# Kernel optimization log

Hardware: AMD Instinct MI355X
Metric: run time of the kernel (lower is better)

## Reference

```python
import jax, jax.numpy as jnp
import numpy as np

N = 1024      # number of atoms
L = 64        # latent_size
VOCAB = 20    # vocab_size (len(ATOM_CATEGORIES))


def _lin(key, fan_in, fan_out):
    # mimic torch nn.Linear init: U(-1/sqrt(fan_in), 1/sqrt(fan_in))
    kw, kb = jax.random.split(key)
    s = 1.0 / np.sqrt(fan_in)
    W = jax.random.uniform(kw, (fan_in, fan_out), minval=-s, maxval=s, dtype=jnp.float32)
    b = jax.random.uniform(kb, (fan_out,), minval=-s, maxval=s, dtype=jnp.float32)
    return W, b


def setup_inputs() -> dict:
    key = jax.random.key(0)
    ks = jax.random.split(key, 9)
    We1, be1 = _lin(ks[3], 2 * L + 1, L)   # mlp_e layer 1
    We2, be2 = _lin(ks[4], L, L)           # mlp_e layer 2
    Wh1, bh1 = _lin(ks[5], L + 1, L)       # mlp_h layer 1
    Wh2, bh2 = _lin(ks[6], L, L)           # mlp_h layer 2
    Wo, bo = _lin(ks[7], L, 1)             # output_mlp
    return {
        "atom_categories": jax.random.randint(ks[0], (N,), 0, VOCAB),
        "atom_coordinates": jax.random.normal(ks[1], (N, 3), dtype=jnp.float32),
        "learnable_matrix": jax.random.normal(ks[2], (VOCAB, L), dtype=jnp.float32),
        "We1": We1, "be1": be1, "We2": We2, "be2": be2,
        "Wh1": Wh1, "bh1": bh1, "Wh2": Wh2, "bh2": bh2,
        "Wo": Wo, "bo": bo,
    }


def reference(atom_categories, atom_coordinates, learnable_matrix,
              We1, be1, We2, be2, Wh1, bh1, Wh2, bh2, Wo, bo):
    Z = atom_coordinates
    # init_H: learnable_matrix.T @ one_hot(cat) == row gather
    H = learnable_matrix[atom_categories]                       # [N, L]

    # pairwise squared distances ||Z_i - Z_j||^2
    d2 = jnp.sum((Z[:, None, :] - Z[None, :, :]) ** 2, axis=-1)  # [N, N]

    # mlp_e layer 1 on concat(H_i, H_j, d2): split We1 to avoid materializing concat
    W1i, W1j, w1z = We1[:L], We1[L:2 * L], We1[2 * L]            # [L,L],[L,L],[L]
    pre_i = H @ W1i                                              # [N, L]
    pre_j = H @ W1j                                              # [N, L]
    h1 = jnp.tanh(pre_i[:, None, :] + pre_j[None, :, :]
                  + d2[:, :, None] * w1z + be1)                  # [N, N, L]
    W_e = jnp.tanh(h1 @ We2 + be2)                               # [N, N, L]

    # V[i] = sum over j != i of sum_l W_e[i,j,l]
    total = jnp.sum(W_e, axis=(1, 2))                            # [N]
    diag = jnp.einsum('iil->i', W_e)                             # [N]
    V = total - diag                                             # [N]

    # mlp_h on concat(H_i, V_i): split Wh1
    hh = jnp.tanh(H @ Wh1[:L] + V[:, None] * Wh1[L] + bh1)       # [N, L]
    newH = jnp.tanh(hh @ Wh2 + bh2)                              # [N, L]

    Hsum = jnp.sum(newH, axis=0)                                 # [L]
    return (Hsum @ Wo + bo)[0]                                   # scalar
```

## Files before the change

### kernel.cpp

```cpp
#include <hip/hip_runtime.h>
#include <hip/hip_bf16.h>


#define N_ATOMS 1024
#define L_DIM 64
#define CSCALE 2.8853900817779268f

typedef _Float16 f16x8 __attribute__((ext_vector_type(8)));
typedef __fp16  fp16x2 __attribute__((ext_vector_type(2)));
typedef float f32x4 __attribute__((ext_vector_type(4)));

__device__ __forceinline__ float tanh_fast(float x) {
    float e = __builtin_amdgcn_exp2f(x * CSCALE);
    float r = __builtin_amdgcn_rcpf(e + 1.0f);
    return fmaf(-2.0f, r, 1.0f);
}

__global__ __launch_bounds__(256) void k_prep(const int* __restrict__ cat,
                                              const float* __restrict__ LM,
                                              const float* __restrict__ We1,
                                              const float* __restrict__ be1,
                                              const float* __restrict__ We2,
                                              const float* __restrict__ be2,
                                              float* __restrict__ H,
                                              float* __restrict__ preI,
                                              float* __restrict__ P3,
                                              float* __restrict__ Vpart,
                                              f16x8* __restrict__ bHg,
                                              f16x8* __restrict__ bLg,
                                              float* __restrict__ biasg,
                                              float* __restrict__ out) {
    int t = threadIdx.x;
    int sub = t >> 6, l = t & 63;
    int i = blockIdx.x * 4 + sub;
    if (blockIdx.x == 0 && t == 0) out[0] = 0.f;
    if (t < 4) Vpart[blockIdx.x * 4 + t] = 0.f;
    __shared__ float hrow[4][L_DIM];
    float hv = LM[cat[i] * L_DIM + l];
    hrow[sub][l] = hv;
    H[i * L_DIM + l] = hv;
    __syncthreads();
    float s1 = 0.f, s2 = 0.f;
#pragma unroll
    for (int m = 0; m < L_DIM; m++) {
        float h = hrow[sub][m];
        s1 = fmaf(h, We1[m * L_DIM + l], s1);
        s2 = fmaf(h, We1[(L_DIM + m) * L_DIM + l], s2);
    }
    preI[i * L_DIM + l] = s1 * CSCALE;
    int cc = i >> 4;
    int Ll = i & 15;
    int quad = (l >> 3) & 3;
    int L = quad * 16 + Ll;
    int g = ((l >> 5) << 1) | ((l >> 2) & 1);
    int e2 = l & 3;
    P3[cc * 1024 + g * 256 + L * 4 + e2] = (s2 + be1[l]) * CSCALE;

    if (blockIdx.x == 0) {
        int nt = t >> 6;
        int lane = t & 63;
        int q2 = lane >> 4, nl2 = lane & 15;
        float psum = 0.f;
#pragma unroll
        for (int kt = 0; kt < 2; kt++) {
            f16x8 hi8, lo8;
#pragma unroll
            for (int e = 0; e < 8; e++) {
                float x = We2[(kt * 32 + q2 * 8 + e) * L_DIM + nt * 16 + nl2];
                psum += x;
                float wp = -2.0f * CSCALE * x;
                _Float16 hi = (_Float16)wp;
                hi8[e] = hi;
                lo8[e] = (_Float16)(wp - (float)hi);
            }
            bHg[(kt * 4 + nt) * 64 + lane] = hi8;
            bLg[(kt * 4 + nt) * 64 + lane] = lo8;
        }
        psum += __shfl_xor(psum, 16);
        psum += __shfl_xor(psum, 32);
        biasg[lane * 4 + nt] = CSCALE * (be2[nt * 16 + nl2] + psum);
    }
}

__global__ __launch_bounds__(256) void k_main(const float* __restrict__ Z,
                                              const float* __restrict__ We1,
                                              const float* __restrict__ preI,
                                              const float* __restrict__ P3,
                                              const f16x8* __restrict__ bHg,
                                              const f16x8* __restrict__ bLg,
                                              const float* __restrict__ biasg,
                                              float* __restrict__ Vpart) {
    int bid = blockIdx.x;
    int i = bid >> 1, half = bid & 1;
    int t = threadIdx.x;
    int lane = t & 63;
    int wave = t >> 6;
    int nlo = lane & 15;
    int quad = lane >> 4;

    __shared__ float d2s[512];
    __shared__ float red[256];
    __shared__ f16x8 bLs[8 * 64];

    float zi0 = Z[i * 3], zi1 = Z[i * 3 + 1], zi2 = Z[i * 3 + 2];
    for (int p = t; p < 512; p += 256) {
        int j = half * 512 + p;
        float a = zi0 - Z[j * 3], b = zi1 - Z[j * 3 + 1], c = zi2 - Z[j * 3 + 2];
        d2s[p] = a * a + b * b + c * c;
    }

    f32x4 aiR[4], wzR[4];
#pragma unroll
    for (int g = 0; g < 4; g++) {
        int mb = ((g >> 1) << 5) + (quad << 3) + ((g & 1) << 2);
        aiR[g] = *(const f32x4*)(preI + i * L_DIM + mb);
        f32x4 wz = *(const f32x4*)(We1 + 2 * L_DIM * L_DIM + mb);
        wzR[g] = wz * CSCALE;
    }

    f16x8 bH[4][2];
#pragma unroll
    for (int nt = 0; nt < 4; nt++) {
        bH[nt][0] = bHg[(0 * 4 + nt) * 64 + lane];
        bH[nt][1] = bHg[(1 * 4 + nt) * 64 + lane];
    }
#pragma unroll
    for (int idx = 0; idx < 2; idx++) {
        int e = wave + idx * 4;
        bLs[e * 64 + lane] = bLg[e * 64 + lane];
    }
    f32x4 bias4 = *(const f32x4*)(biasg + lane * 4);

    const float* Pbase = P3 + (half * 32 + wave * 8) * 1024 + lane * 4;
    f32x4 p0 = *(const f32x4*)(Pbase + 0 * 256) + aiR[0];
    f32x4 p1 = *(const f32x4*)(Pbase + 1 * 256) + aiR[1];
    f32x4 p2 = *(const f32x4*)(Pbase + 2 * 256) + aiR[2];
    f32x4 p3 = *(const f32x4*)(Pbase + 3 * 256) + aiR[3];

    __syncthreads();

    f32x4 Vr4 = {0.f, 0.f, 0.f, 0.f};
    for (int k = 0; k < 8; k++) {
        float d2 = d2s[(wave * 8 + k) * 16 + nlo];
        f32x4 d2v = {d2, d2, d2, d2};

        f32x4 z0 = p0 + d2v * wzR[0];
        f32x4 z1 = p1 + d2v * wzR[1];
        f32x4 z2 = p2 + d2v * wzR[2];
        f32x4 z3 = p3 + d2v * wzR[3];
        f32x4 ex0, ex1, ex2, ex3;
#pragma unroll
        for (int e = 0; e < 4; e++) {
            ex0[e] = __builtin_amdgcn_exp2f(z0[e]);
            ex1[e] = __builtin_amdgcn_exp2f(z1[e]);
            ex2[e] = __builtin_amdgcn_exp2f(z2[e]);
            ex3[e] = __builtin_amdgcn_exp2f(z3[e]);
        }
        ex0 += 1.0f; ex1 += 1.0f; ex2 += 1.0f; ex3 += 1.0f;
        f32x4 r0, r1, r2, r3;
#pragma unroll
        for (int e = 0; e < 4; e++) {
            r0[e] = __builtin_amdgcn_rcpf(ex0[e]);
            r1[e] = __builtin_amdgcn_rcpf(ex1[e]);
            r2[e] = __builtin_amdgcn_rcpf(ex2[e]);
            r3[e] = __builtin_amdgcn_rcpf(ex3[e]);
        }
        union { f16x8 v; fp16x2 h2[4]; } u0, u1;
        u0.h2[0] = __builtin_amdgcn_cvt_pkrtz(r0[0], r0[1]);
        u0.h2[1] = __builtin_amdgcn_cvt_pkrtz(r0[2], r0[3]);
        u0.h2[2] = __builtin_amdgcn_cvt_pkrtz(r1[0], r1[1]);
        u0.h2[3] = __builtin_amdgcn_cvt_pkrtz(r1[2], r1[3]);
        u1.h2[0] = __builtin_amdgcn_cvt_pkrtz(r2[0], r2[1]);
        u1.h2[1] = __builtin_amdgcn_cvt_pkrtz(r2[2], r2[3]);
        u1.h2[2] = __builtin_amdgcn_cvt_pkrtz(r3[0], r3[1]);
        u1.h2[3] = __builtin_amdgcn_cvt_pkrtz(r3[2], r3[3]);
        f16x8 aH0 = u0.v, aH1 = u1.v;

        if (k < 7) {
            const float* nb = Pbase + (k + 1) * 1024;
            p0 = *(const f32x4*)(nb + 0 * 256) + aiR[0];
            p1 = *(const f32x4*)(nb + 1 * 256) + aiR[1];
            p2 = *(const f32x4*)(nb + 2 * 256) + aiR[2];
            p3 = *(const f32x4*)(nb + 3 * 256) + aiR[3];
        }

#pragma unroll
        for (int nt = 0; nt < 4; nt++) {
            f16x8 bl0 = bLs[(0 * 4 + nt) * 64 + lane];
            f16x8 bl1 = bLs[(1 * 4 + nt) * 64 + lane];
            f32x4 acc = {bias4[nt], bias4[nt], bias4[nt], bias4[nt]};
            acc = __builtin_amdgcn_mfma_f32_16x16x32_f16(aH0, bH[nt][0], acc, 0, 0, 0);
            acc = __builtin_amdgcn_mfma_f32_16x16x32_f16(aH0, bl0, acc, 0, 0, 0);
            acc = __builtin_amdgcn_mfma_f32_16x16x32_f16(aH1, bH[nt][1], acc, 0, 0, 0);
            acc = __builtin_amdgcn_mfma_f32_16x16x32_f16(aH1, bl1, acc, 0, 0, 0);
            f32x4 ev;
#pragma unroll
            for (int r4 = 0; r4 < 4; r4++) ev[r4] = __builtin_amdgcn_exp2f(acc[r4]);
            ev += 1.0f;
            f32x4 rv;
#pragma unroll
            for (int r4 = 0; r4 < 4; r4++) rv[r4] = __builtin_amdgcn_rcpf(ev[r4]);
            Vr4 += rv;
        }
    }

    red[t] = Vr4[0] + Vr4[1] + Vr4[2] + Vr4[3];
    __syncthreads();
    if (t < 64) {
        float r = red[t] + red[t + 64] + red[t + 128] + red[t + 192];
#pragma unroll
        for (int o = 32; o > 0; o >>= 1) r += __shfl_xor(r, o);
        if (t == 0) atomicAdd(Vpart + i, r);
    }
}

__global__ __launch_bounds__(256) void k_post(const float* __restrict__ preI,
                                              const float* __restrict__ P3,
                                              const float* __restrict__ H,
                                              const float* __restrict__ We2,
                                              const float* __restrict__ be2,
                                              const float* __restrict__ Wh1,
                                              const float* __restrict__ bh1,
                                              const float* __restrict__ Wh2,
                                              const float* __restrict__ bh2,
                                              const float* __restrict__ Wo,
                                              const float* __restrict__ bo,
                                              const float* __restrict__ Vpart,
                                              float* __restrict__ out) {
    int t = threadIdx.x;
    int sub = t >> 6, lane = t & 63;
    int i = blockIdx.x * 4 + sub;
    __shared__ float dgt[4][L_DIM];
    __shared__ float hrow_s[4][L_DIM];
    __shared__ float hh_s[4][L_DIM];

    float Rall = Vpart[i];
    int cc = i >> 4, Ll = i & 15;
    int q2 = (lane >> 3) & 3;
    int g = ((lane >> 5) << 1) | ((lane >> 2) & 1);
    float z = preI[i * L_DIM + lane] + P3[cc * 1024 + g * 256 + (q2 * 16 + Ll) * 4 + (lane & 3)];
    float rr = __builtin_amdgcn_rcpf(__builtin_amdgcn_exp2f(z) + 1.0f);
    dgt[sub][lane] = fmaf(-2.0f, rr, 1.0f);
    hrow_s[sub][lane] = H[i * L_DIM + lane];
    __syncthreads();

    float S = be2[lane];
#pragma unroll
    for (int m = 0; m < L_DIM; m++) S = fmaf(dgt[sub][m], We2[m * L_DIM + lane], S);
    float rd = __builtin_amdgcn_rcpf(__builtin_amdgcn_exp2f(S * CSCALE) + 1.0f);
#pragma unroll
    for (int o = 32; o > 0; o >>= 1) rd += __shfl_xor(rd, o);
    float V = fmaf(-2.0f, Rall - rd, (float)(1023 * L_DIM));
    float s = 0.f;
#pragma unroll
    for (int m = 0; m < L_DIM; m++) s = fmaf(hrow_s[sub][m], Wh1[m * L_DIM + lane], s);
    s = fmaf(V, Wh1[L_DIM * L_DIM + lane], s) + bh1[lane];
    hh_s[sub][lane] = tanh_fast(s);
    __syncthreads();

    float s2 = 0.f;
#pragma unroll
    for (int m = 0; m < L_DIM; m++) s2 = fmaf(hh_s[sub][m], Wh2[m * L_DIM + lane], s2);
    float nh = tanh_fast(s2 + bh2[lane]);
    float w = nh * Wo[lane];
#pragma unroll
    for (int o = 32; o > 0; o >>= 1) w += __shfl_down(w, o);
    if (lane == 0) atomicAdd(out, w + (i == 0 ? bo[0] : 0.f));
}

extern "C" void kernel_launch(void* const* d_in, const int* in_sizes, int n_in,
                              void* d_out, int out_size, void* d_ws, size_t ws_size,
                              hipStream_t stream) {
    const int*   cat = (const int*)  d_in[0];
    const float* Z   = (const float*)d_in[1];
    const float* LM  = (const float*)d_in[2];
    const float* We1 = (const float*)d_in[3];
    const float* be1 = (const float*)d_in[4];
    const float* We2 = (const float*)d_in[5];
    const float* be2 = (const float*)d_in[6];
    const float* Wh1 = (const float*)d_in[7];
    const float* bh1 = (const float*)d_in[8];
    const float* Wh2 = (const float*)d_in[9];
    const float* bh2 = (const float*)d_in[10];
    const float* Wo  = (const float*)d_in[11];
    const float* bo  = (const float*)d_in[12];
    float* out = (float*)d_out;

    float* ws    = (float*)d_ws;
    float* H     = ws;
    float* preI  = H     + N_ATOMS * L_DIM;
    float* P3    = preI  + N_ATOMS * L_DIM;
    float* Vpart = P3    + N_ATOMS * L_DIM;
    float* biasg = Vpart + N_ATOMS;
    f16x8* bHg   = (f16x8*)(biasg + 256);
    f16x8* bLg   = bHg + 8 * 64;

    k_prep<<<N_ATOMS / 4, 256, 0, stream>>>(cat, LM, We1, be1, We2, be2,
                                            H, preI, P3, Vpart, bHg, bLg, biasg, out);
    k_main<<<N_ATOMS * 2, 256, 0, stream>>>(Z, We1, preI, P3, bHg, bLg, biasg, Vpart);
    k_post<<<N_ATOMS / 4, 256, 0, stream>>>(preI, P3, H, We2, be2,
                                            Wh1, bh1, Wh2, bh2, Wo, bo, Vpart, out);
}
```

Before: 137.3 us.

## Fuse main and post kernels via last-block-done counter, use per-category projection table

Replaces the three-kernel pipeline with a tiny setup kernel plus one fused kernel. The per-atom j-side projection is rebuilt as a 20-row per-category table in shared memory, indexed by atom category, instead of a 1024-row global P3 array. The per-atom MLP tail now runs in whichever of the two half-blocks finishes second, detected with an atomic done counter, which removes the k_post launch. In exchange every block recomputes the category table and the i-side projection (about 1.3K FMAs per thread of redundant work), and correctness relies on atomics and threadfence ordering.

New measurement: 239.7 us. 74.5% more time.

```diff
diff --git a/kernel.cpp b/kernel.cpp
--- a/kernel.cpp
+++ b/kernel.cpp
@@ -5,6 +5,7 @@
 #define N_ATOMS 1024
 #define L_DIM 64
 #define CSCALE 2.8853900817779268f
+#define T2LD 68
 
 typedef _Float16 f16x8 __attribute__((ext_vector_type(8)));
 typedef __fp16  fp16x2 __attribute__((ext_vector_type(2)));
@@ -16,46 +17,15 @@
     return fmaf(-2.0f, r, 1.0f);
 }
 
-__global__ __launch_bounds__(256) void k_prep(const int* __restrict__ cat,
-                                              const float* __restrict__ LM,
-                                              const float* __restrict__ We1,
-                                              const float* __restrict__ be1,
-                                              const float* __restrict__ We2,
+__global__ __launch_bounds__(256) void k_pre0(const float* __restrict__ We2,
                                               const float* __restrict__ be2,
-                                              float* __restrict__ H,
-                                              float* __restrict__ preI,
-                                              float* __restrict__ P3,
-                                              float* __restrict__ Vpart,
                                               f16x8* __restrict__ bHg,
                                               f16x8* __restrict__ bLg,
                                               float* __restrict__ biasg,
+                                              float* __restrict__ Vpart,
+                                              int* __restrict__ done,
                                               float* __restrict__ out) {
     int t = threadIdx.x;
-    int sub = t >> 6, l = t & 63;
-    int i = blockIdx.x * 4 + sub;
-    if (blockIdx.x == 0 && t == 0) out[0] = 0.f;
-    if (t < 4) Vpart[blockIdx.x * 4 + t] = 0.f;
-    __shared__ float hrow[4][L_DIM];
-    float hv = LM[cat[i] * L_DIM + l];
-    hrow[sub][l] = hv;
-    H[i * L_DIM + l] = hv;
-    __syncthreads();
-    float s1 = 0.f, s2 = 0.f;
-#pragma unroll
-    for (int m = 0; m < L_DIM; m++) {
-        float h = hrow[sub][m];
-        s1 = fmaf(h, We1[m * L_DIM + l], s1);
-        s2 = fmaf(h, We1[(L_DIM + m) * L_DIM + l], s2);
-    }
-    preI[i * L_DIM + l] = s1 * CSCALE;
-    int cc = i >> 4;
-    int Ll = i & 15;
-    int quad = (l >> 3) & 3;
-    int L = quad * 16 + Ll;
-    int g = ((l >> 5) << 1) | ((l >> 2) & 1);
-    int e2 = l & 3;
-    P3[cc * 1024 + g * 256 + L * 4 + e2] = (s2 + be1[l]) * CSCALE;
-
     if (blockIdx.x == 0) {
         int nt = t >> 6;
         int lane = t & 63;
@@ -79,17 +49,33 @@
         psum += __shfl_xor(psum, 16);
         psum += __shfl_xor(psum, 32);
         biasg[lane * 4 + nt] = CSCALE * (be2[nt * 16 + nl2] + psum);
+        if (t == 0) out[0] = 0.f;
+    } else {
+        int idx = (blockIdx.x - 1) * 256 + t;
+        if (idx < N_ATOMS) Vpart[idx] = 0.f;
+        else done[idx - N_ATOMS] = 0;
     }
 }
 
-__global__ __launch_bounds__(256) void k_main(const float* __restrict__ Z,
-                                              const float* __restrict__ We1,
-                                              const float* __restrict__ preI,
-                                              const float* __restrict__ P3,
-                                              const f16x8* __restrict__ bHg,
-                                              const f16x8* __restrict__ bLg,
-                                              const float* __restrict__ biasg,
-                                              float* __restrict__ Vpart) {
+__global__ __launch_bounds__(256) void k_fused(const int* __restrict__ cat,
+                                               const float* __restrict__ Z,
+                                               const float* __restrict__ LM,
+                                               const float* __restrict__ We1,
+                                               const float* __restrict__ be1,
+                                               const float* __restrict__ We2,
+                                               const float* __restrict__ be2,
+                                               const f16x8* __restrict__ bHg,
+                                               const f16x8* __restrict__ bLg,
+                                               const float* __restrict__ biasg,
+                                               const float* __restrict__ Wh1,
+                                               const float* __restrict__ bh1,
+                                               const float* __restrict__ Wh2,
+                                               const float* __restrict__ bh2,
+                                               const float* __restrict__ Wo,
+                                               const float* __restrict__ bo,
+                                               float* __restrict__ Vpart,
+                                               int* __restrict__ done,
+                                               float* __restrict__ out) {
     int bid = blockIdx.x;
     int i = bid >> 1, half = bid & 1;
     int t = threadIdx.x;
@@ -101,21 +87,38 @@
     __shared__ float d2s[512];
     __shared__ float red[256];
     __shared__ f16x8 bLs[8 * 64];
+    __shared__ float T2s[20 * T2LD];
+    __shared__ float preIs[L_DIM];
+    __shared__ int   cats[512];
+    __shared__ float dgt[L_DIM];
+    __shared__ float hhs[L_DIM];
+    __shared__ float RallS;
+    __shared__ int   winflag;
 
     float zi0 = Z[i * 3], zi1 = Z[i * 3 + 1], zi2 = Z[i * 3 + 2];
     for (int p = t; p < 512; p += 256) {
         int j = half * 512 + p;
+        cats[p] = cat[j];
         float a = zi0 - Z[j * 3], b = zi1 - Z[j * 3 + 1], c = zi2 - Z[j * 3 + 2];
         d2s[p] = a * a + b * b + c * c;
     }
 
-    f32x4 aiR[4], wzR[4];
-#pragma unroll
-    for (int g = 0; g < 4; g++) {
-        int mb = ((g >> 1) << 5) + (quad << 3) + ((g & 1) << 2);
-        aiR[g] = *(const f32x4*)(preI + i * L_DIM + mb);
-        f32x4 wz = *(const f32x4*)(We1 + 2 * L_DIM * L_DIM + mb);
-        wzR[g] = wz * CSCALE;
+#pragma unroll
+    for (int r = 0; r < 5; r++) {
+        int c = wave + 4 * r;
+        float s = 0.f;
+#pragma unroll
+        for (int m = 0; m < L_DIM; m++)
+            s = fmaf(LM[c * L_DIM + m], We1[(L_DIM + m) * L_DIM + lane], s);
+        T2s[c * T2LD + lane] = (s + be1[lane]) * CSCALE;
+    }
+    int ci = cat[i];
+    if (t < 64) {
+        float s = 0.f;
+#pragma unroll
+        for (int m = 0; m < L_DIM; m++)
+            s = fmaf(LM[ci * L_DIM + m], We1[m * L_DIM + t], s);
+        preIs[t] = s * CSCALE;
     }
 
     f16x8 bH[4][2];
@@ -131,13 +134,33 @@
     }
     f32x4 bias4 = *(const f32x4*)(biasg + lane * 4);
 
-    const float* Pbase = P3 + (half * 32 + wave * 8) * 1024 + lane * 4;
-    f32x4 p0 = *(const f32x4*)(Pbase + 0 * 256) + aiR[0];
-    f32x4 p1 = *(const f32x4*)(Pbase + 1 * 256) + aiR[1];
-    f32x4 p2 = *(const f32x4*)(Pbase + 2 * 256) + aiR[2];
-    f32x4 p3 = *(const f32x4*)(Pbase + 3 * 256) + aiR[3];
+    int mbs[4];
+    f32x4 wzR[4];
+#pragma unroll
+    for (int g = 0; g < 4; g++) {
+        int mb = ((g >> 1) << 5) + (quad << 3) + ((g & 1) << 2);
+        mbs[g] = mb;
+        f32x4 wz = *(const f32x4*)(We1 + 2 * L_DIM * L_DIM + mb);
+        wzR[g] = wz * CSCALE;
+    }
 
     __syncthreads();
+
+    f32x4 aiR[4];
+#pragma unroll
+    for (int g = 0; g < 4; g++) aiR[g] = *(const f32x4*)(preIs + mbs[g]);
+
+    {
+        int sc = cats[(wave * 8 + 0) * 16 + nlo];
+        const float* Tr = T2s + sc * T2LD;
+        (void)Tr;
+    }
+    int sc0 = cats[(wave * 8) * 16 + nlo];
+    const float* Tr0 = T2s + sc0 * T2LD;
+    f32x4 p0 = *(const f32x4*)(Tr0 + mbs[0]) + aiR[0];
+    f32x4 p1 = *(const f32x4*)(Tr0 + mbs[1]) + aiR[1];
+    f32x4 p2 = *(const f32x4*)(Tr0 + mbs[2]) + aiR[2];
+    f32x4 p3 = *(const f32x4*)(Tr0 + mbs[3]) + aiR[3];
 
     f32x4 Vr4 = {0.f, 0.f, 0.f, 0.f};
     for (int k = 0; k < 8; k++) {
@@ -177,11 +200,12 @@
         f16x8 aH0 = u0.v, aH1 = u1.v;
 
         if (k < 7) {
-            const float* nb = Pbase + (k + 1) * 1024;
-            p0 = *(const f32x4*)(nb + 0 * 256) + aiR[0];
-            p1 = *(const f32x4*)(nb + 1 * 256) + aiR[1];
-            p2 = *(const f32x4*)(nb + 2 * 256) + aiR[2];
-            p3 = *(const f32x4*)(nb + 3 * 256) + aiR[3];
+            int sc = cats[(wave * 8 + k + 1) * 16 + nlo];
+            const float* Tr = T2s + sc * T2LD;
+            p0 = *(const f32x4*)(Tr + mbs[0]) + aiR[0];
+            p1 = *(const f32x4*)(Tr + mbs[1]) + aiR[1];
+            p2 = *(const f32x4*)(Tr + mbs[2]) + aiR[2];
+            p3 = *(const f32x4*)(Tr + mbs[3]) + aiR[3];
         }
 
 #pragma unroll
@@ -206,66 +230,59 @@
 
     red[t] = Vr4[0] + Vr4[1] + Vr4[2] + Vr4[3];
     __syncthreads();
+
     if (t < 64) {
         float r = red[t] + red[t + 64] + red[t + 128] + red[t + 192];
 #pragma unroll
         for (int o = 32; o > 0; o >>= 1) r += __shfl_xor(r, o);
-        if (t == 0) atomicAdd(Vpart + i, r);
-    }
-}
-
-__global__ __launch_bounds__(256) void k_post(const float* __restrict__ preI,
-                                              const float* __restrict__ P3,
-                                              const float* __restrict__ H,
-                                              const float* __restrict__ We2,
-                                              const float* __restrict__ be2,
-                                              const float* __restrict__ Wh1,
-                                              const float* __restrict__ bh1,
-                                              const float* __restrict__ Wh2,
-                                              const float* __restrict__ bh2,
-                                              const float* __restrict__ Wo,
-                                              const float* __restrict__ bo,
-                                              const float* __restrict__ Vpart,
-                                              float* __restrict__ out) {
-    int t = threadIdx.x;
-    int sub = t >> 6, lane = t & 63;
-    int i = blockIdx.x * 4 + sub;
-    __shared__ float dgt[4][L_DIM];
-    __shared__ float hrow_s[4][L_DIM];
-    __shared__ float hh_s[4][L_DIM];
-
-    float Rall = Vpart[i];
-    int cc = i >> 4, Ll = i & 15;
-    int q2 = (lane >> 3) & 3;
-    int g = ((lane >> 5) << 1) | ((lane >> 2) & 1);
-    float z = preI[i * L_DIM + lane] + P3[cc * 1024 + g * 256 + (q2 * 16 + Ll) * 4 + (lane & 3)];
-    float rr = __builtin_amdgcn_rcpf(__builtin_amdgcn_exp2f(z) + 1.0f);
-    dgt[sub][lane] = fmaf(-2.0f, rr, 1.0f);
-    hrow_s[sub][lane] = H[i * L_DIM + lane];
+        if (t == 0) {
+            atomicAdd(Vpart + i, r);
+            __threadfence();
+            int old = atomicAdd(done + i, 1);
+            if (old == 1) {
+                __threadfence();
+                RallS = atomicAdd(Vpart + i, 0.0f);
+                winflag = 1;
+            } else {
+                winflag = 0;
+            }
+        }
+    }
     __syncthreads();
 
-    float S = be2[lane];
-#pragma unroll
-    for (int m = 0; m < L_DIM; m++) S = fmaf(dgt[sub][m], We2[m * L_DIM + lane], S);
-    float rd = __builtin_amdgcn_rcpf(__builtin_amdgcn_exp2f(S * CSCALE) + 1.0f);
-#pragma unroll
-    for (int o = 32; o > 0; o >>= 1) rd += __shfl_xor(rd, o);
-    float V = fmaf(-2.0f, Rall - rd, (float)(1023 * L_DIM));
-    float s = 0.f;
-#pragma unroll
-    for (int m = 0; m < L_DIM; m++) s = fmaf(hrow_s[sub][m], Wh1[m * L_DIM + lane], s);
-    s = fmaf(V, Wh1[L_DIM * L_DIM + lane], s) + bh1[lane];
-    hh_s[sub][lane] = tanh_fast(s);
-    __syncthreads();
-
-    float s2 = 0.f;
-#pragma unroll
-    for (int m = 0; m < L_DIM; m++) s2 = fmaf(hh_s[sub][m], Wh2[m * L_DIM + lane], s2);
-    float nh = tanh_fast(s2 + bh2[lane]);
-    float w = nh * Wo[lane];
-#pragma unroll
-    for (int o = 32; o > 0; o >>= 1) w += __shfl_down(w, o);
-    if (lane == 0) atomicAdd(out, w + (i == 0 ? bo[0] : 0.f));
+    if (winflag) {
+        if (t < 64) {
+            float z = preIs[t] + T2s[ci * T2LD + t];
+            float rr = __builtin_amdgcn_rcpf(__builtin_amdgcn_exp2f(z) + 1.0f);
+            dgt[t] = fmaf(-2.0f, rr, 1.0f);
+        }
+        __syncthreads();
+        if (t < 64) {
+            float S = be2[t];
+#pragma unroll
+            for (int m = 0; m < L_DIM; m++) S = fmaf(dgt[m], We2[m * L_DIM + t], S);
+            float rd = __builtin_amdgcn_rcpf(__builtin_amdgcn_exp2f(S * CSCALE) + 1.0f);
+#pragma unroll
+            for (int o = 32; o > 0; o >>= 1) rd += __shfl_xor(rd, o);
+            float V = fmaf(-2.0f, RallS - rd, (float)(1023 * L_DIM));
+            float s = 0.f;
+#pragma unroll
+            for (int m = 0; m < L_DIM; m++) s = fmaf(LM[ci * L_DIM + m], Wh1[m * L_DIM + t], s);
+            s = fmaf(V, Wh1[L_DIM * L_DIM + t], s) + bh1[t];
+            hhs[t] = tanh_fast(s);
+        }
+        __syncthreads();
+        if (t < 64) {
+            float s2 = 0.f;
+#pragma unroll
+            for (int m = 0; m < L_DIM; m++) s2 = fmaf(hhs[m], Wh2[m * L_DIM + t], s2);
+            float nh = tanh_fast(s2 + bh2[t]);
+            float w = nh * Wo[t];
+#pragma unroll
+            for (int o = 32; o > 0; o >>= 1) w += __shfl_down(w, o);
+            if (t == 0) atomicAdd(out, w + (i == 0 ? bo[0] : 0.f));
+        }
+    }
 }
 
 extern "C" void kernel_launch(void* const* d_in, const int* in_sizes, int n_in,
@@ -287,17 +304,15 @@
     float* out = (float*)d_out;
 
     float* ws    = (float*)d_ws;
-    float* H     = ws;
-    float* preI  = H     + N_ATOMS * L_DIM;
-    float* P3    = preI  + N_ATOMS * L_DIM;
-    float* Vpart = P3    + N_ATOMS * L_DIM;
-    float* biasg = Vpart + N_ATOMS;
-    f16x8* bHg   = (f16x8*)(biasg + 256);
+    float* Vpart = ws;
+    int*   done  = (int*)(ws + N_ATOMS);
+    float* biasg = ws + 2 * N_ATOMS;
+    f16x8* bHg   = (f16x8*)(ws + 2 * N_ATOMS + 256);
     f16x8* bLg   = bHg + 8 * 64;
 
-    k_prep<<<N_ATOMS / 4, 256, 0, stream>>>(cat, LM, We1, be1, We2, be2,
-                                            H, preI, P3, Vpart, bHg, bLg, biasg, out);
-    k_main<<<N_ATOMS * 2, 256, 0, stream>>>(Z, We1, preI, P3, bHg, bLg, biasg, Vpart);
-    k_post<<<N_ATOMS / 4, 256, 0, stream>>>(preI, P3, H, We2, be2,
-                                            Wh1, bh1, Wh2, bh2, Wo, bo, Vpart, out);
+    k_pre0<<<9, 256, 0, stream>>>(We2, be2, bHg, bLg, biasg, Vpart, done, out);
+    k_fused<<<N_ATOMS * 2, 256, 0, stream>>>(cat, Z, LM, We1, be1, We2, be2,
+                                             bHg, bLg, biasg,
+                                             Wh1, bh1, Wh2, bh2, Wo, bo,
+                                             Vpart, done, out);
 }
```

## Fuse post-processing into main kernel via last-block-done atomic counter

Applied to the files above, without the earlier changes.

Removes the k_post launch by having the second of two blocks finishing each atom (detected with an atomic done counter after a threadfence) run the per-atom mlp_h and output reduction inside k_main. This saves one kernel launch and its tail/launch gap. In exchange it adds atomics and a fence per block, a serial tail of one-wave work on the winning block, and extra shared memory and registers in k_main that could lower occupancy.

New measurement: 150.8 us. 1.1x slower.

```diff
diff --git a/kernel.cpp b/kernel.cpp
--- a/kernel.cpp
+++ b/kernel.cpp
@@ -26,6 +26,7 @@
                                               float* __restrict__ preI,
                                               float* __restrict__ P3,
                                               float* __restrict__ Vpart,
+                                              int* __restrict__ done,
                                               f16x8* __restrict__ bHg,
                                               f16x8* __restrict__ bLg,
                                               float* __restrict__ biasg,
@@ -34,7 +35,10 @@
     int sub = t >> 6, l = t & 63;
     int i = blockIdx.x * 4 + sub;
     if (blockIdx.x == 0 && t == 0) out[0] = 0.f;
-    if (t < 4) Vpart[blockIdx.x * 4 + t] = 0.f;
+    if (t < 4) {
+        Vpart[blockIdx.x * 4 + t] = 0.f;
+        done[blockIdx.x * 4 + t] = 0;
+    }
     __shared__ float hrow[4][L_DIM];
     float hv = LM[cat[i] * L_DIM + l];
     hrow[sub][l] = hv;
@@ -89,7 +93,18 @@
                                               const f16x8* __restrict__ bHg,
                                               const f16x8* __restrict__ bLg,
                                               const float* __restrict__ biasg,
-                                              float* __restrict__ Vpart) {
+                                              const float* __restrict__ H,
+                                              const float* __restrict__ We2,
+                                              const float* __restrict__ be2,
+                                              const float* __restrict__ Wh1,
+                                              const float* __restrict__ bh1,
+                                              const float* __restrict__ Wh2,
+                                              const float* __restrict__ bh2,
+                                              const float* __restrict__ Wo,
+                                              const float* __restrict__ bo,
+                                              float* __restrict__ Vpart,
+                                              int* __restrict__ done,
+                                              float* __restrict__ out) {
     int bid = blockIdx.x;
     int i = bid >> 1, half = bid & 1;
     int t = threadIdx.x;
@@ -101,6 +116,11 @@
     __shared__ float d2s[512];
     __shared__ float red[256];
     __shared__ f16x8 bLs[8 * 64];
+    __shared__ float dgt[L_DIM];
+    __shared__ float hrow_s[L_DIM];
+    __shared__ float hhs[L_DIM];
+    __shared__ float RallS;
+    __shared__ int   winflag;
 
     float zi0 = Z[i * 3], zi1 = Z[i * 3 + 1], zi2 = Z[i * 3 + 2];
     for (int p = t; p < 512; p += 256) {
@@ -206,66 +226,62 @@
 
     red[t] = Vr4[0] + Vr4[1] + Vr4[2] + Vr4[3];
     __syncthreads();
+
     if (t < 64) {
         float r = red[t] + red[t + 64] + red[t + 128] + red[t + 192];
 #pragma unroll
         for (int o = 32; o > 0; o >>= 1) r += __shfl_xor(r, o);
-        if (t == 0) atomicAdd(Vpart + i, r);
-    }
-}
-
-__global__ __launch_bounds__(256) void k_post(const float* __restrict__ preI,
-                                              const float* __restrict__ P3,
-                                              const float* __restrict__ H,
-                                              const float* __restrict__ We2,
-                                              const float* __restrict__ be2,
-                                              const float* __restrict__ Wh1,
-                                              const float* __restrict__ bh1,
-                                              const float* __restrict__ Wh2,
-                                              const float* __restrict__ bh2,
-                                              const float* __restrict__ Wo,
-                                              const float* __restrict__ bo,
-                                              const float* __restrict__ Vpart,
-                                              float* __restrict__ out) {
-    int t = threadIdx.x;
-    int sub = t >> 6, lane = t & 63;
-    int i = blockIdx.x * 4 + sub;
-    __shared__ float dgt[4][L_DIM];
-    __shared__ float hrow_s[4][L_DIM];
-    __shared__ float hh_s[4][L_DIM];
-
-    float Rall = Vpart[i];
-    int cc = i >> 4, Ll = i & 15;
-    int q2 = (lane >> 3) & 3;
-    int g = ((lane >> 5) << 1) | ((lane >> 2) & 1);
-    float z = preI[i * L_DIM + lane] + P3[cc * 1024 + g * 256 + (q2 * 16 + Ll) * 4 + (lane & 3)];
-    float rr = __builtin_amdgcn_rcpf(__builtin_amdgcn_exp2f(z) + 1.0f);
-    dgt[sub][lane] = fmaf(-2.0f, rr, 1.0f);
-    hrow_s[sub][lane] = H[i * L_DIM + lane];
+        if (t == 0) {
+            atomicAdd(Vpart + i, r);
+            __threadfence();
+            int old = atomicAdd(done + i, 1);
+            if (old == 1) {
+                RallS = atomicAdd(Vpart + i, 0.0f);
+                winflag = 1;
+            } else {
+                winflag = 0;
+            }
+        }
+    }
     __syncthreads();
 
-    float S = be2[lane];
-#pragma unroll
-    for (int m = 0; m < L_DIM; m++) S = fmaf(dgt[sub][m], We2[m * L_DIM + lane], S);
-    float rd = __builtin_amdgcn_rcpf(__builtin_amdgcn_exp2f(S * CSCALE) + 1.0f);
-#pragma unroll
-    for (int o = 32; o > 0; o >>= 1) rd += __shfl_xor(rd, o);
-    float V = fmaf(-2.0f, Rall - rd, (float)(1023 * L_DIM));
-    float s = 0.f;
-#pragma unroll
-    for (int m = 0; m < L_DIM; m++) s = fmaf(hrow_s[sub][m], Wh1[m * L_DIM + lane], s);
-    s = fmaf(V, Wh1[L_DIM * L_DIM + lane], s) + bh1[lane];
-    hh_s[sub][lane] = tanh_fast(s);
-    __syncthreads();
-
-    float s2 = 0.f;
-#pragma unroll
-    for (int m = 0; m < L_DIM; m++) s2 = fmaf(hh_s[sub][m], Wh2[m * L_DIM + lane], s2);
-    float nh = tanh_fast(s2 + bh2[lane]);
-    float w = nh * Wo[lane];
-#pragma unroll
-    for (int o = 32; o > 0; o >>= 1) w += __shfl_down(w, o);
-    if (lane == 0) atomicAdd(out, w + (i == 0 ? bo[0] : 0.f));
+    if (winflag) {
+        if (t < 64) {
+            int cc = i >> 4, Ll = i & 15;
+            int q2 = (t >> 3) & 3;
+            int g = ((t >> 5) << 1) | ((t >> 2) & 1);
+            float z = preI[i * L_DIM + t] + P3[cc * 1024 + g * 256 + (q2 * 16 + Ll) * 4 + (t & 3)];
+            float rr = __builtin_amdgcn_rcpf(__builtin_amdgcn_exp2f(z) + 1.0f);
+            dgt[t] = fmaf(-2.0f, rr, 1.0f);
+            hrow_s[t] = H[i * L_DIM + t];
+        }
+        __syncthreads();
+        if (t < 64) {
+            float S = be2[t];
+#pragma unroll
+            for (int m = 0; m < L_DIM; m++) S = fmaf(dgt[m], We2[m * L_DIM + t], S);
+            float rd = __builtin_amdgcn_rcpf(__builtin_amdgcn_exp2f(S * CSCALE) + 1.0f);
+#pragma unroll
+            for (int o = 32; o > 0; o >>= 1) rd += __shfl_xor(rd, o);
+            float V = fmaf(-2.0f, RallS - rd, (float)(1023 * L_DIM));
+            float s = 0.f;
+#pragma unroll
+            for (int m = 0; m < L_DIM; m++) s = fmaf(hrow_s[m], Wh1[m * L_DIM + t], s);
+            s = fmaf(V, Wh1[L_DIM * L_DIM + t], s) + bh1[t];
+            hhs[t] = tanh_fast(s);
+        }
+        __syncthreads();
+        if (t < 64) {
+            float s2 = 0.f;
+#pragma unroll
+            for (int m = 0; m < L_DIM; m++) s2 = fmaf(hhs[m], Wh2[m * L_DIM + t], s2);
+            float nh = tanh_fast(s2 + bh2[t]);
+            float w = nh * Wo[t];
+#pragma unroll
+            for (int o = 32; o > 0; o >>= 1) w += __shfl_down(w, o);
+            if (t == 0) atomicAdd(out, w + (i == 0 ? bo[0] : 0.f));
+        }
+    }
 }
 
 extern "C" void kernel_launch(void* const* d_in, const int* in_sizes, int n_in,
@@ -291,13 +307,14 @@
     float* preI  = H     + N_ATOMS * L_DIM;
     float* P3    = preI  + N_ATOMS * L_DIM;
     float* Vpart = P3    + N_ATOMS * L_DIM;
-    float* biasg = Vpart + N_ATOMS;
+    int*   done  = (int*)(Vpart + N_ATOMS);
+    float* biasg = (float*)(done + N_ATOMS);
     f16x8* bHg   = (f16x8*)(biasg + 256);
     f16x8* bLg   = bHg + 8 * 64;
 
     k_prep<<<N_ATOMS / 4, 256, 0, stream>>>(cat, LM, We1, be1, We2, be2,
-                                            H, preI, P3, Vpart, bHg, bLg, biasg, out);
-    k_main<<<N_ATOMS * 2, 256, 0, stream>>>(Z, We1, preI, P3, bHg, bLg, biasg, Vpart);
-    k_post<<<N_ATOMS / 4, 256, 0, stream>>>(preI, P3, H, We2, be2,
-                                            Wh1, bh1, Wh2, bh2, Wo, bo, Vpart, out);
+                                            H, preI, P3, Vpart, done, bHg, bLg, biasg, out);
+    k_main<<<N_ATOMS * 2, 256, 0, stream>>>(Z, We1, preI, P3, bHg, bLg, biasg,
+                                            H, We2, be2, Wh1, bh1, Wh2, bh2, Wo, bo,
+                                            Vpart, done, out);
 }
```
